# Kernel optimization log

Hardware: AMD Instinct MI355X
Metric: run time of the kernel (lower is better)

The kernel has to match this reference:

```python
import jax, jax.numpy as jnp
import numpy as np

NODE_FEATURES = 256
HIDDEN = 32
N_NODES = 100000
N_EDGES = 3200000


def _glorot(key, shape):
    fan_in, fan_out = shape[-2], shape[-1]
    lim = (6.0 / (fan_in + fan_out)) ** 0.5
    return jax.random.uniform(key, shape, jnp.float32, -lim, lim)


def setup_inputs() -> dict:
    key = jax.random.key(0)
    ks = jax.random.split(key, 12)
    in_cat = NODE_FEATURES + HIDDEN  # DConv input is cat([X, H])
    x = jax.random.normal(ks[0], (N_NODES, NODE_FEATURES), jnp.float32)
    edge_index = jax.random.randint(ks[1], (2, N_EDGES), 0, N_NODES, jnp.int64)
    return {
        "x": x,
        "edge_index": edge_index,
        # DConv weights have shape (2, K=1, in, out); squeeze K -> (2, in, out)
        "w_z": _glorot(ks[2], (2, in_cat, HIDDEN)),
        "b_z": jnp.zeros((HIDDEN,), jnp.float32),
        "w_r": _glorot(ks[3], (2, in_cat, HIDDEN)),
        "b_r": jnp.zeros((HIDDEN,), jnp.float32),
        "w_h": _glorot(ks[4], (2, in_cat, HIDDEN)),
        "b_h": jnp.zeros((HIDDEN,), jnp.float32),
        # fc head, stored as [in, out]
        "fc1_w": _glorot(ks[5], (HIDDEN, HIDDEN)),
        "fc1_b": jnp.zeros((HIDDEN,), jnp.float32),
        "fc2_w": _glorot(ks[6], (HIDDEN, 1)),
        "fc2_b": jnp.zeros((1,), jnp.float32),
    }


def _dconv_k1(inp, w, b):
    # K=1 DConv: only the k=0 Chebyshev term for both diffusion directions,
    # i.e. no propagation over edges. H = X @ W_out + X @ W_in + bias.
    return inp @ (w[0] + w[1]) + b


def reference(x, edge_index, w_z, b_z, w_r, b_r, w_h, b_h, fc1_w, fc1_b, fc2_w, fc2_b):
    n = x.shape[0]
    h0 = jnp.zeros((n, HIDDEN), x.dtype)  # DCRNN called with H=None -> zeros
    xh0 = jnp.concatenate([x, h0], axis=1)  # [N, F+H]
    z = jax.nn.sigmoid(_dconv_k1(xh0, w_z, b_z))  # update gate
    r = jax.nn.sigmoid(_dconv_k1(xh0, w_r, b_r))  # reset gate
    xrh = jnp.concatenate([x, r * h0], axis=1)
    h_tilde = jnp.tanh(_dconv_k1(xrh, w_h, b_h))
    h = z * h0 + (1.0 - z) * h_tilde  # [N, 32]
    # fc head: Linear-ReLU-Dropout(eval=identity)-Linear-Sigmoid
    hidden = jax.nn.relu(h @ fc1_w + fc1_b)
    out = jax.nn.sigmoid(hidden @ fc2_w + fc2_b)  # [N, 1]
    return out
```

## Files before the change

### kernel.cpp

```cpp
#include <hip/hip_runtime.h>
#include <hip/hip_bf16.h>


#define NF    256
#define TILE  32
#define WPB   4
#define MB    (TILE * WPB)
#define NTHR  256
#define BGRP  1040
#define HSTR  36

typedef __attribute__((ext_vector_type(8)))  short  short8;
typedef __attribute__((ext_vector_type(16))) float  floatx16;

__device__ __forceinline__ unsigned f2bf(float f) {
    __hip_bfloat16 h = __float2bfloat16(f);
    return (unsigned)*(unsigned short*)&h;
}
__device__ __forceinline__ float fast_sigmoid(float v) {
    return 1.0f / (1.0f + __expf(-v));
}
__device__ __forceinline__ float fast_tanh(float v) {
    return 1.0f - 2.0f / (1.0f + __expf(2.0f * v));
}

__global__ void prep_W(const float* __restrict__ wz,
                       const float* __restrict__ wh,
                       unsigned short* __restrict__ Wf)
{
    int idx = blockIdx.x * blockDim.x + threadIdx.x;
    if (idx >= NF * 64) return;
    int j    = idx & 7;
    int lane = (idx >> 3) & 63;
    int nt   = (idx >> 9) & 1;
    int kt   = idx >> 10;
    int k = kt * 16 + (lane >> 5) * 8 + j;
    int o = nt * 32 + (lane & 31);
    const int PLANE = 288 * 32;
    float v;
    if (o < 32) v = wz[k * 32 + o]        + wz[PLANE + k * 32 + o];
    else        v = wh[k * 32 + (o - 32)] + wh[PLANE + k * 32 + (o - 32)];
    Wf[idx] = (unsigned short)f2bf(v);
}

__global__ void __launch_bounds__(NTHR, 3)
rgcn_main(const float* __restrict__ x,
          const unsigned short* __restrict__ Wf,
          const float* __restrict__ bz,
          const float* __restrict__ bh,
          const float* __restrict__ fc1w,
          const float* __restrict__ fc1b,
          const float* __restrict__ fc2w,
          const float* __restrict__ fc2b,
          float* __restrict__ out,
          int n_nodes)
{
    __shared__ __align__(16) char SB[32 * BGRP];
    __shared__ float Hs[WPB * TILE * HSTR];

    const int tid   = threadIdx.x;
    const int lane  = tid & 63;
    const int wave  = tid >> 6;
    const int node0 = blockIdx.x * MB;

    {
        const uint4* src = (const uint4*)Wf;
#pragma unroll
        for (int i = 0; i < 8; ++i) {
            int q = i * NTHR + tid;
            uint4 v = src[q];
            *(uint4*)(SB + (q >> 6) * BGRP + (q & 63) * 16) = v;
        }
    }
    __syncthreads();

    const int m  = lane & 31;
    int gn_a = node0 + wave * TILE + m;
    if (gn_a >= n_nodes) gn_a = n_nodes - 1;
    const float* xr = x + (size_t)gn_a * NF + (lane >> 5) * 8;

    floatx16 acc0 = {};
    floatx16 acc1 = {};

    float4 bufA[8], bufB[8];
    const char* bl = SB + lane * 16;

#pragma unroll
    for (int t = 0; t < 8; ++t)
        bufA[t] = *(const float4*)(xr + (t >> 1) * 16 + (t & 1) * 4);
    __builtin_amdgcn_sched_barrier(0);

#pragma unroll
    for (int c = 0; c < 4; ++c) {
        if (c < 3) {
            float4* nb = ((c & 1) == 0) ? bufB : bufA;
            const float* xc = xr + (c + 1) * 64;
#pragma unroll
            for (int t = 0; t < 8; ++t)
                nb[t] = *(const float4*)(xc + (t >> 1) * 16 + (t & 1) * 4);
            __builtin_amdgcn_sched_barrier(0);
        }
        const float4* cb = ((c & 1) == 0) ? bufA : bufB;
#pragma unroll
        for (int kt = 0; kt < 4; ++kt) {
            float4 v0 = cb[kt * 2];
            float4 v1 = cb[kt * 2 + 1];
            int g = (c * 4 + kt) * 2;
            uint4 b0u = *(const uint4*)(bl + (size_t)g * BGRP);
            uint4 b1u = *(const uint4*)(bl + (size_t)(g + 1) * BGRP);
            union { short8 s; unsigned u[4]; } a, b0, b1;
            a.u[0] = f2bf(v0.x) | (f2bf(v0.y) << 16);
            a.u[1] = f2bf(v0.z) | (f2bf(v0.w) << 16);
            a.u[2] = f2bf(v1.x) | (f2bf(v1.y) << 16);
            a.u[3] = f2bf(v1.z) | (f2bf(v1.w) << 16);
            b0.u[0] = b0u.x; b0.u[1] = b0u.y; b0.u[2] = b0u.z; b0.u[3] = b0u.w;
            b1.u[0] = b1u.x; b1.u[1] = b1u.y; b1.u[2] = b1u.z; b1.u[3] = b1u.w;
            acc0 = __builtin_amdgcn_mfma_f32_32x32x16_bf16(a.s, b0.s, acc0, 0, 0, 0);
            acc1 = __builtin_amdgcn_mfma_f32_32x32x16_bf16(a.s, b1.s, acc1, 0, 0, 0);
        }
    }

    float* Hw = Hs + wave * TILE * HSTR;
    const int nc = lane & 31;
    const float bzn = bz[nc];
    const float bhn = bh[nc];
#pragma unroll
    for (int r = 0; r < 16; ++r) {
        int row = (r & 3) + 8 * (r >> 2) + 4 * (lane >> 5);
        float z = fast_sigmoid(acc0[r] + bzn);
        float t = fast_tanh   (acc1[r] + bhn);
        Hw[row * HSTR + nc] = (1.0f - z) * t;
    }
    asm volatile("s_waitcnt lgkmcnt(0)" ::: "memory");

    const int nl   = lane & 31;
    const int half = lane >> 5;
    const float* hp = Hw + nl * HSTR;
    float h[32];
#pragma unroll
    for (int q = 0; q < 8; ++q) {
        float4 v = *(const float4*)(hp + q * 4);
        h[q * 4 + 0] = v.x; h[q * 4 + 1] = v.y;
        h[q * 4 + 2] = v.z; h[q * 4 + 3] = v.w;
    }
    float part = 0.0f;
    for (int jj = 0; jj < 16; ++jj) {
        int j = (half << 4) + jj;
        float s = fc1b[j];
#pragma unroll
        for (int o = 0; o < 32; ++o)
            s = fmaf(h[o], fc1w[o * 32 + j], s);
        part = fmaf(fmaxf(s, 0.0f), fc2w[j], part);
    }
    part += __shfl_xor(part, 32);
    if (half == 0) {
        int gn = node0 + wave * TILE + nl;
        if (gn < n_nodes)
            out[gn] = fast_sigmoid(part + fc2b[0]);
    }
}

extern "C" void kernel_launch(void* const* d_in, const int* in_sizes, int n_in,
                              void* d_out, int out_size, void* d_ws, size_t ws_size,
                              hipStream_t stream) {
    const float* x    = (const float*)d_in[0];
    const float* wz   = (const float*)d_in[2];
    const float* bz   = (const float*)d_in[3];
    const float* wh   = (const float*)d_in[6];
    const float* bh   = (const float*)d_in[7];
    const float* fc1w = (const float*)d_in[8];
    const float* fc1b = (const float*)d_in[9];
    const float* fc2w = (const float*)d_in[10];
    const float* fc2b = (const float*)d_in[11];
    float* out = (float*)d_out;
    unsigned short* Wf = (unsigned short*)d_ws;

    const int n = in_sizes[0] / NF;

    prep_W<<<(NF * 64 + 255) / 256, 256, 0, stream>>>(wz, wh, Wf);
    rgcn_main<<<(n + MB - 1) / MB, NTHR, 0, stream>>>(
        x, Wf, bz, bh, fc1w, fc1b, fc2w, fc2b, out, n);
}
```

Baseline: 203.5 us.

## Stream X tiles into LDS via async global_load_lds with double buffering

Replaces the register-staged float4 loads of x with direct global-to-LDS DMA (global_load_lds), double-buffered in per-wave XOR-swizzled LDS tiles, with the MFMA loop split into 16 chunks gated by vmcnt waits. Weight staging into LDS also uses the DMA path, and the epilogue H buffer reuses the A staging area with a swizzled layout instead of padded strides. The aim is to cut VGPR pressure, raise occupancy and overlap memory with compute. The trade-off is a shallower prefetch depth (two chunks) and more wait points, which could expose more latency.

Measured after the change: 205.5 us. No clear change (+1.0%).

```diff
diff --git a/kernel.cpp b/kernel.cpp
--- a/kernel.cpp
+++ b/kernel.cpp
@@ -2,13 +2,13 @@
 #include <hip/hip_bf16.h>
 
 
-#define NF    256
-#define TILE  32
-#define WPB   4
-#define MB    (TILE * WPB)
-#define NTHR  256
-#define BGRP  1040
-#define HSTR  36
+#define NF     256
+#define TILE   32
+#define WPB    4
+#define MB     (TILE * WPB)
+#define NTHR   256
+#define NCHUNK 16
+#define ABUF   2048
 
 typedef __attribute__((ext_vector_type(8)))  short  short8;
 typedef __attribute__((ext_vector_type(16))) float  floatx16;
@@ -22,6 +22,12 @@
 }
 __device__ __forceinline__ float fast_tanh(float v) {
     return 1.0f - 2.0f / (1.0f + __expf(2.0f * v));
+}
+__device__ __forceinline__ void dma16(const void* g, void* l) {
+    __builtin_amdgcn_global_load_lds(
+        (const __attribute__((address_space(1))) unsigned int*)g,
+        (__attribute__((address_space(3))) unsigned int*)l,
+        16, 0, 0);
 }
 
 __global__ void prep_W(const float* __restrict__ wz,
@@ -55,91 +61,99 @@
           float* __restrict__ out,
           int n_nodes)
 {
-    __shared__ __align__(16) char SB[32 * BGRP];
-    __shared__ float Hs[WPB * TILE * HSTR];
+    __shared__ __align__(16) char SA [WPB * 2 * ABUF];
+    __shared__ __align__(16) char SBf[32 * 1024];
 
     const int tid   = threadIdx.x;
     const int lane  = tid & 63;
     const int wave  = tid >> 6;
-    const int node0 = blockIdx.x * MB;
+    const int node0 = blockIdx.x * MB + wave * TILE;
 
     {
-        const uint4* src = (const uint4*)Wf;
+        const char* wsrc = (const char*)Wf;
 #pragma unroll
         for (int i = 0; i < 8; ++i) {
-            int q = i * NTHR + tid;
-            uint4 v = src[q];
-            *(uint4*)(SB + (q >> 6) * BGRP + (q & 63) * 16) = v;
+            int g = wave * 8 + i;
+            dma16(wsrc + (size_t)g * 1024 + lane * 16, SBf + g * 1024);
         }
     }
+
+    const int nc  = lane & 31;
+    const float bzn = bz[nc];
+    const float bhn = bh[nc];
+
+    asm volatile("s_waitcnt vmcnt(0)" ::: "memory");
     __syncthreads();
 
-    const int m  = lane & 31;
-    int gn_a = node0 + wave * TILE + m;
-    if (gn_a >= n_nodes) gn_a = n_nodes - 1;
-    const float* xr = x + (size_t)gn_a * NF + (lane >> 5) * 8;
+    const int srow = lane >> 2;
+    const int slot = (lane & 3) ^ ((lane >> 3) & 3);
+    int r0 = node0 + srow;       if (r0 >= n_nodes) r0 = n_nodes - 1;
+    int r1 = node0 + 16 + srow;  if (r1 >= n_nodes) r1 = n_nodes - 1;
+    const char* a0p = (const char*)x + (size_t)r0 * (NF * 4) + slot * 16;
+    const char* a1p = (const char*)x + (size_t)r1 * (NF * 4) + slot * 16;
+    char* aw = SA + wave * (2 * ABUF);
+
+    const int m   = lane & 31;
+    const int rsw = (m >> 1) & 3;
+    const int s0  = (lane >> 5) * 2;
+    const int ra0 = m * 64 + (((s0    ) ^ rsw) << 4);
+    const int ra1 = m * 64 + (((s0 + 1) ^ rsw) << 4);
+    const char* bl = SBf + lane * 16;
+
+    dma16(a0p +  0, aw);          dma16(a1p +  0, aw + 1024);
+    dma16(a0p + 64, aw + ABUF);   dma16(a1p + 64, aw + ABUF + 1024);
 
     floatx16 acc0 = {};
     floatx16 acc1 = {};
 
-    float4 bufA[8], bufB[8];
-    const char* bl = SB + lane * 16;
+#pragma unroll
+    for (int c = 0; c < NCHUNK; ++c) {
+        if (c < NCHUNK - 1) asm volatile("s_waitcnt vmcnt(2)" ::: "memory");
+        else                asm volatile("s_waitcnt vmcnt(0)" ::: "memory");
+        __builtin_amdgcn_sched_barrier(0);
 
-#pragma unroll
-    for (int t = 0; t < 8; ++t)
-        bufA[t] = *(const float4*)(xr + (t >> 1) * 16 + (t & 1) * 4);
-    __builtin_amdgcn_sched_barrier(0);
+        char* ab = aw + (c & 1) * ABUF;
+        float4 f0 = *(const float4*)(ab + ra0);
+        float4 f1 = *(const float4*)(ab + ra1);
+        uint4  vb0 = *(const uint4*)(bl + (size_t)(2 * c    ) * 1024);
+        uint4  vb1 = *(const uint4*)(bl + (size_t)(2 * c + 1) * 1024);
 
-#pragma unroll
-    for (int c = 0; c < 4; ++c) {
-        if (c < 3) {
-            float4* nb = ((c & 1) == 0) ? bufB : bufA;
-            const float* xc = xr + (c + 1) * 64;
-#pragma unroll
-            for (int t = 0; t < 8; ++t)
-                nb[t] = *(const float4*)(xc + (t >> 1) * 16 + (t & 1) * 4);
+        union { short8 s; unsigned u[4]; } A, B0, B1;
+        A.u[0] = f2bf(f0.x) | (f2bf(f0.y) << 16);
+        A.u[1] = f2bf(f0.z) | (f2bf(f0.w) << 16);
+        A.u[2] = f2bf(f1.x) | (f2bf(f1.y) << 16);
+        A.u[3] = f2bf(f1.z) | (f2bf(f1.w) << 16);
+        B0.u[0] = vb0.x; B0.u[1] = vb0.y; B0.u[2] = vb0.z; B0.u[3] = vb0.w;
+        B1.u[0] = vb1.x; B1.u[1] = vb1.y; B1.u[2] = vb1.z; B1.u[3] = vb1.w;
+
+        acc0 = __builtin_amdgcn_mfma_f32_32x32x16_bf16(A.s, B0.s, acc0, 0, 0, 0);
+        acc1 = __builtin_amdgcn_mfma_f32_32x32x16_bf16(A.s, B1.s, acc1, 0, 0, 0);
+
+        if (c + 2 < NCHUNK) {
             __builtin_amdgcn_sched_barrier(0);
-        }
-        const float4* cb = ((c & 1) == 0) ? bufA : bufB;
-#pragma unroll
-        for (int kt = 0; kt < 4; ++kt) {
-            float4 v0 = cb[kt * 2];
-            float4 v1 = cb[kt * 2 + 1];
-            int g = (c * 4 + kt) * 2;
-            uint4 b0u = *(const uint4*)(bl + (size_t)g * BGRP);
-            uint4 b1u = *(const uint4*)(bl + (size_t)(g + 1) * BGRP);
-            union { short8 s; unsigned u[4]; } a, b0, b1;
-            a.u[0] = f2bf(v0.x) | (f2bf(v0.y) << 16);
-            a.u[1] = f2bf(v0.z) | (f2bf(v0.w) << 16);
-            a.u[2] = f2bf(v1.x) | (f2bf(v1.y) << 16);
-            a.u[3] = f2bf(v1.z) | (f2bf(v1.w) << 16);
-            b0.u[0] = b0u.x; b0.u[1] = b0u.y; b0.u[2] = b0u.z; b0.u[3] = b0u.w;
-            b1.u[0] = b1u.x; b1.u[1] = b1u.y; b1.u[2] = b1u.z; b1.u[3] = b1u.w;
-            acc0 = __builtin_amdgcn_mfma_f32_32x32x16_bf16(a.s, b0.s, acc0, 0, 0, 0);
-            acc1 = __builtin_amdgcn_mfma_f32_32x32x16_bf16(a.s, b1.s, acc1, 0, 0, 0);
+            dma16(a0p + (size_t)(c + 2) * 64, ab);
+            dma16(a1p + (size_t)(c + 2) * 64, ab + 1024);
         }
     }
 
-    float* Hw = Hs + wave * TILE * HSTR;
-    const int nc = lane & 31;
-    const float bzn = bz[nc];
-    const float bhn = bh[nc];
+    float* Hw = (float*)aw;
 #pragma unroll
     for (int r = 0; r < 16; ++r) {
         int row = (r & 3) + 8 * (r >> 2) + 4 * (lane >> 5);
         float z = fast_sigmoid(acc0[r] + bzn);
         float t = fast_tanh   (acc1[r] + bhn);
-        Hw[row * HSTR + nc] = (1.0f - z) * t;
+        int boff = row * 128 + ((((nc >> 2) ^ (row & 7)) << 4) | ((nc & 3) << 2));
+        *(float*)((char*)Hw + boff) = (1.0f - z) * t;
     }
     asm volatile("s_waitcnt lgkmcnt(0)" ::: "memory");
 
     const int nl   = lane & 31;
     const int half = lane >> 5;
-    const float* hp = Hw + nl * HSTR;
     float h[32];
 #pragma unroll
     for (int q = 0; q < 8; ++q) {
-        float4 v = *(const float4*)(hp + q * 4);
+        int boff = nl * 128 + ((q ^ (nl & 7)) << 4);
+        float4 v = *(const float4*)((char*)Hw + boff);
         h[q * 4 + 0] = v.x; h[q * 4 + 1] = v.y;
         h[q * 4 + 2] = v.z; h[q * 4 + 3] = v.w;
     }
@@ -154,7 +168,7 @@
     }
     part += __shfl_xor(part, 32);
     if (half == 0) {
-        int gn = node0 + wave * TILE + nl;
+        int gn = node0 + nl;
         if (gn < n_nodes)
             out[gn] = fast_sigmoid(part + fc2b[0]);
     }
```
